# Performance work log

Hardware: AMD Instinct MI355X
Metric: run time of the kernel (lower is better)

Reference implementation:

```python
import jax, jax.numpy as jnp
import numpy as np

OUT, IN = 4096, 4096
BLOCK = 32
NBLK = IN // BLOCK  # 128


def setup_inputs() -> dict:
    key = jax.random.key(0)
    k1, k2, k3 = jax.random.split(key, 3)
    x = jax.random.normal(k1, (2, 2048, IN), dtype=jnp.float32)
    # per-block scales (GGUF stores fp16 scales; small magnitude typical)
    scales = jax.random.normal(k2, (OUT, NBLK), dtype=jnp.float32) * 0.01
    # int8 codes stored as unsigned 0..255; signed value = code - 128
    codes = jax.random.randint(k3, (OUT, NBLK, BLOCK), 0, 256, dtype=jnp.int32)
    return {"x": x, "scales": scales, "codes": codes}


def dequantize_q8_0(scales, codes):
    # scales: [out, nblk], codes: [out, nblk, 32] unsigned -> signed int8 semantics
    signed = codes.astype(jnp.float32) - 128.0
    w = scales[:, :, None] * signed            # [out, nblk, 32]
    return w.reshape(OUT, IN)                   # [out, in]


def reference(x, scales, codes):
    weight = dequantize_q8_0(scales, codes)     # [out, in]
    # nn.functional.linear: y = x @ weight.T
    return jnp.einsum("bsi,oi->bso", x, weight)
```

## Files before the change

### kernel.cpp

```cpp
#include <hip/hip_runtime.h>
#include <stdint.h>


#define M_DIM 4096
#define N_DIM 4096
#define K_DIM 4096
#define NT    64

typedef __attribute__((ext_vector_type(8))) short bf16x8;
typedef __attribute__((ext_vector_type(4))) float f32x4;

__device__ __forceinline__ unsigned short f32_to_bf16_rne(float f) {
    unsigned u = __float_as_uint(f);
    u += 0x7fffu + ((u >> 16) & 1u);
    return (unsigned short)(u >> 16);
}

__device__ __forceinline__ void load_lds16(const void* g, void* l) {
    __builtin_amdgcn_global_load_lds(
        (const __attribute__((address_space(1))) unsigned int*)g,
        (__attribute__((address_space(3))) unsigned int*)l, 16, 0, 0);
}

__global__ __launch_bounds__(256) void prologue_kernel(
        const int* __restrict__ codes, const float* __restrict__ scales,
        unsigned short* __restrict__ W,
        const float* __restrict__ x, unsigned short* __restrict__ xb) {
    const int bid = blockIdx.x;
    if (bid < 8192) {
        const int tid = bid * 256 + threadIdx.x;
        const int o   = tid >> 9;
        const int blk = (tid & 511) >> 2;
        const float s = scales[o * 128 + blk];
        const int4 c0 = ((const int4*)codes)[(size_t)tid * 2];
        const int4 c1 = ((const int4*)codes)[(size_t)tid * 2 + 1];
        union { unsigned short u[8]; uint4 v; } p;
        p.u[0] = f32_to_bf16_rne(s * (float)(c0.x - 128));
        p.u[1] = f32_to_bf16_rne(s * (float)(c0.y - 128));
        p.u[2] = f32_to_bf16_rne(s * (float)(c0.z - 128));
        p.u[3] = f32_to_bf16_rne(s * (float)(c0.w - 128));
        p.u[4] = f32_to_bf16_rne(s * (float)(c1.x - 128));
        p.u[5] = f32_to_bf16_rne(s * (float)(c1.y - 128));
        p.u[6] = f32_to_bf16_rne(s * (float)(c1.z - 128));
        p.u[7] = f32_to_bf16_rne(s * (float)(c1.w - 128));
        ((uint4*)W)[tid] = p.v;
    } else {
        const int tid = (bid - 8192) * 256 + threadIdx.x;
        const float4 f0 = ((const float4*)x)[(size_t)tid * 2];
        const float4 f1 = ((const float4*)x)[(size_t)tid * 2 + 1];
        union { unsigned short u[8]; uint4 v; } p;
        p.u[0] = f32_to_bf16_rne(f0.x); p.u[1] = f32_to_bf16_rne(f0.y);
        p.u[2] = f32_to_bf16_rne(f0.z); p.u[3] = f32_to_bf16_rne(f0.w);
        p.u[4] = f32_to_bf16_rne(f1.x); p.u[5] = f32_to_bf16_rne(f1.y);
        p.u[6] = f32_to_bf16_rne(f1.z); p.u[7] = f32_to_bf16_rne(f1.w);
        ((uint4*)xb)[tid] = p.v;
    }
}

#define BAR()   asm volatile("s_barrier" ::: "memory")
#define LGKM0() asm volatile("s_waitcnt lgkmcnt(0)" ::: "memory")
#define VMC(N)  asm volatile("s_waitcnt vmcnt(" #N ")" ::: "memory")

__global__ __launch_bounds__(512, 2) void gemm_8phase(
        const unsigned short* __restrict__ A,
        const unsigned short* __restrict__ B,
        float* __restrict__ C) {
    __shared__ unsigned short sA[2][2][256 * 32];
    __shared__ unsigned short sB[2][2][256 * 32];

    const int tid  = threadIdx.x;
    const int wave = tid >> 6;
    const int lane = tid & 63;

    const int bid  = blockIdx.x;
    const int xcd  = bid & 7;
    const int slot = bid >> 3;
    const int m0 = ((xcd >> 2) * 8 + (slot >> 2)) * 256;
    const int n0 = ((xcd & 3) * 4 + (slot & 3)) * 256;

    const int srow   = lane >> 2;
    const int schunk = (lane & 3) ^ ((lane >> 3) & 3);
    const unsigned short* Ag = A + (size_t)(m0 + wave * 32 + srow) * K_DIM + schunk * 8;
    const unsigned short* Bg = B + (size_t)(n0 + wave * 32 + srow) * K_DIM + schunk * 8;
    const int ldsW = wave * 1024;

    const int frow = lane & 15;
    const int quad = lane >> 4;
    const int wm = wave >> 2;
    const int wn = wave & 3;
    const int cswz = (quad ^ ((frow >> 1) & 3)) * 8;
    const int aOff = (wm * 128 + frow) * 32 + cswz;
    const int bOff = (wn * 64 + frow) * 32 + cswz;

    f32x4 acc[8][4] = {};
    bf16x8 a[8], b0, b1, b2, b3;

#define STG_A(BUF, KH, KT) do { \
        const unsigned short* s_ = Ag + (size_t)(KT) * 64 + (KH) * 32; \
        load_lds16(s_,                       &sA[BUF][KH][ldsW]); \
        load_lds16(s_ + (size_t)16 * K_DIM,  &sA[BUF][KH][ldsW + 512]); \
    } while (0)
#define STG_B(BUF, KH, KT) do { \
        const unsigned short* s_ = Bg + (size_t)(KT) * 64 + (KH) * 32; \
        load_lds16(s_,                       &sB[BUF][KH][ldsW]); \
        load_lds16(s_ + (size_t)16 * K_DIM,  &sB[BUF][KH][ldsW + 512]); \
    } while (0)
#define RD_A(BUF, KH) do { _Pragma("unroll") \
        for (int mt_ = 0; mt_ < 8; ++mt_) \
            a[mt_] = *(const bf16x8*)&sA[BUF][KH][aOff + mt_ * 512]; \
    } while (0)
#define RD_B2(BUF, KH, NB, R0, R1) do { \
        R0 = *(const bf16x8*)&sB[BUF][KH][bOff + (NB) * 512]; \
        R1 = *(const bf16x8*)&sB[BUF][KH][bOff + (NB + 1) * 512]; \
    } while (0)
#define MM2(NC, R0, R1) do { _Pragma("unroll") \
        for (int mt_ = 0; mt_ < 8; ++mt_) { \
            acc[mt_][NC]     = __builtin_amdgcn_mfma_f32_16x16x32_bf16(a[mt_], R0, acc[mt_][NC],     0, 0, 0); \
            acc[mt_][NC + 1] = __builtin_amdgcn_mfma_f32_16x16x32_bf16(a[mt_], R1, acc[mt_][NC + 1], 0, 0, 0); \
        } } while (0)

#define KTILE(BUF, OBUF, T, I1, I2, I3, I4, VMF) do { \
         \
        RD_A(BUF, 0); RD_B2(BUF, 0, 0, b0, b1); \
        if (I1) { STG_B(OBUF, 1, (T) + 1); } \
        BAR(); LGKM0(); __builtin_amdgcn_s_setprio(1); \
        MM2(0, b0, b1); \
        __builtin_amdgcn_s_setprio(0); BAR(); \
         \
        RD_B2(BUF, 0, 2, b2, b3); \
        if (I2) { STG_A(BUF, 0, (T) + 2); } \
        BAR(); LGKM0(); __builtin_amdgcn_s_setprio(1); \
        MM2(2, b2, b3); \
        __builtin_amdgcn_s_setprio(0); BAR(); \
         \
        RD_A(BUF, 1); RD_B2(BUF, 1, 0, b0, b1); \
        if (I3) { STG_B(BUF, 0, (T) + 2); } \
        BAR(); LGKM0(); __builtin_amdgcn_s_setprio(1); \
        MM2(0, b0, b1); \
        __builtin_amdgcn_s_setprio(0); BAR(); \
         \
        RD_B2(BUF, 1, 2, b2, b3); \
        if (I4) { STG_A(BUF, 1, (T) + 2); } \
        BAR(); LGKM0(); __builtin_amdgcn_s_setprio(1); \
        MM2(2, b2, b3); \
        __builtin_amdgcn_s_setprio(0); \
        VMF; BAR(); \
    } while (0)

    STG_A(0, 0, 0); STG_B(0, 0, 0); STG_A(0, 1, 0); STG_B(0, 1, 0);
    STG_A(1, 0, 1); STG_B(1, 0, 1); STG_A(1, 1, 1);
    VMC(6); BAR();

#pragma unroll 1
    for (int t2 = 0; t2 < 31; ++t2) {
        const int t = t2 * 2;
        KTILE(0, 1, t,     1, 1, 1, 1, VMC(6));
        KTILE(1, 0, t + 1, 1, 1, 1, 1, VMC(6));
    }
    KTILE(0, 1, 62, 1, 0, 0, 0, VMC(0));
    KTILE(1, 0, 63, 0, 0, 0, 0, (void)0);

    const size_t crow0 = (size_t)(m0 + wm * 128 + quad * 4);
    const int    ccol  = n0 + wn * 64 + frow;
#pragma unroll
    for (int mt = 0; mt < 8; ++mt)
#pragma unroll
        for (int nt = 0; nt < 4; ++nt)
#pragma unroll
            for (int r = 0; r < 4; ++r)
                C[(crow0 + mt * 16 + r) * N_DIM + ccol + nt * 16] = acc[mt][nt][r];

#undef STG_A
#undef STG_B
#undef RD_A
#undef RD_B2
#undef MM2
#undef KTILE
}

extern "C" void kernel_launch(void* const* d_in, const int* in_sizes, int n_in,
                              void* d_out, int out_size, void* d_ws, size_t ws_size,
                              hipStream_t stream) {
    const float* x      = (const float*)d_in[0];
    const float* scales = (const float*)d_in[1];
    const int*   codes  = (const int*)d_in[2];
    float* y = (float*)d_out;

    unsigned short* Wb = (unsigned short*)d_ws;
    unsigned short* xb = (unsigned short*)((char*)d_ws + (size_t)N_DIM * K_DIM * 2);

    prologue_kernel<<<16384, 256, 0, stream>>>(codes, scales, Wb, x, xb);

    gemm_8phase<<<256, 512, 0, stream>>>(xb, Wb, y);
}
```

Before: 293.4 us.

## Split MFMA phases by M-half to cut A-fragment registers; halve prologue work per thread

The GEMM inner phases now hold 4 A fragments and 4 B fragments instead of 8 A fragments plus 4 B fragments. Each phase computes a 4x4 MFMA block over one M-half, and the staging order of A/B tiles across phases is rearranged to match. The intent is to lower VGPR pressure and balance LDS reads per phase, at the cost of re-reading the B fragments per K-half. The prologue is also changed to process 4 elements per thread with twice as many blocks, which gives more parallelism but narrower 8-byte stores.

```diff
diff --git a/kernel.cpp b/kernel.cpp
--- a/kernel.cpp
+++ b/kernel.cpp
@@ -5,7 +5,6 @@
 #define M_DIM 4096
 #define N_DIM 4096
 #define K_DIM 4096
-#define NT    64
 
 typedef __attribute__((ext_vector_type(8))) short bf16x8;
 typedef __attribute__((ext_vector_type(4))) float f32x4;
@@ -27,33 +26,23 @@
         unsigned short* __restrict__ W,
         const float* __restrict__ x, unsigned short* __restrict__ xb) {
     const int bid = blockIdx.x;
-    if (bid < 8192) {
+    if (bid < 16384) {
         const int tid = bid * 256 + threadIdx.x;
-        const int o   = tid >> 9;
-        const int blk = (tid & 511) >> 2;
-        const float s = scales[o * 128 + blk];
-        const int4 c0 = ((const int4*)codes)[(size_t)tid * 2];
-        const int4 c1 = ((const int4*)codes)[(size_t)tid * 2 + 1];
-        union { unsigned short u[8]; uint4 v; } p;
-        p.u[0] = f32_to_bf16_rne(s * (float)(c0.x - 128));
-        p.u[1] = f32_to_bf16_rne(s * (float)(c0.y - 128));
-        p.u[2] = f32_to_bf16_rne(s * (float)(c0.z - 128));
-        p.u[3] = f32_to_bf16_rne(s * (float)(c0.w - 128));
-        p.u[4] = f32_to_bf16_rne(s * (float)(c1.x - 128));
-        p.u[5] = f32_to_bf16_rne(s * (float)(c1.y - 128));
-        p.u[6] = f32_to_bf16_rne(s * (float)(c1.z - 128));
-        p.u[7] = f32_to_bf16_rne(s * (float)(c1.w - 128));
-        ((uint4*)W)[tid] = p.v;
+        const float s = scales[tid >> 3];
+        const int4 c  = ((const int4*)codes)[tid];
+        union { unsigned short u[4]; uint2 v; } p;
+        p.u[0] = f32_to_bf16_rne(s * (float)(c.x - 128));
+        p.u[1] = f32_to_bf16_rne(s * (float)(c.y - 128));
+        p.u[2] = f32_to_bf16_rne(s * (float)(c.z - 128));
+        p.u[3] = f32_to_bf16_rne(s * (float)(c.w - 128));
+        ((uint2*)W)[tid] = p.v;
     } else {
-        const int tid = (bid - 8192) * 256 + threadIdx.x;
-        const float4 f0 = ((const float4*)x)[(size_t)tid * 2];
-        const float4 f1 = ((const float4*)x)[(size_t)tid * 2 + 1];
-        union { unsigned short u[8]; uint4 v; } p;
-        p.u[0] = f32_to_bf16_rne(f0.x); p.u[1] = f32_to_bf16_rne(f0.y);
-        p.u[2] = f32_to_bf16_rne(f0.z); p.u[3] = f32_to_bf16_rne(f0.w);
-        p.u[4] = f32_to_bf16_rne(f1.x); p.u[5] = f32_to_bf16_rne(f1.y);
-        p.u[6] = f32_to_bf16_rne(f1.z); p.u[7] = f32_to_bf16_rne(f1.w);
-        ((uint4*)xb)[tid] = p.v;
+        const int tid = (bid - 16384) * 256 + threadIdx.x;
+        const float4 f = ((const float4*)x)[tid];
+        union { unsigned short u[4]; uint2 v; } p;
+        p.u[0] = f32_to_bf16_rne(f.x); p.u[1] = f32_to_bf16_rne(f.y);
+        p.u[2] = f32_to_bf16_rne(f.z); p.u[3] = f32_to_bf16_rne(f.w);
+        ((uint2*)xb)[tid] = p.v;
     }
 }
 
@@ -93,7 +82,7 @@
     const int bOff = (wn * 64 + frow) * 32 + cswz;
 
     f32x4 acc[8][4] = {};
-    bf16x8 a[8], b0, b1, b2, b3;
+    bf16x8 a[4], b[4];
 
 #define STG_A(BUF, KH, KT) do { \
         const unsigned short* s_ = Ag + (size_t)(KT) * 64 + (KH) * 32; \
@@ -105,50 +94,51 @@
         load_lds16(s_,                       &sB[BUF][KH][ldsW]); \
         load_lds16(s_ + (size_t)16 * K_DIM,  &sB[BUF][KH][ldsW + 512]); \
     } while (0)
-#define RD_A(BUF, KH) do { _Pragma("unroll") \
-        for (int mt_ = 0; mt_ < 8; ++mt_) \
-            a[mt_] = *(const bf16x8*)&sA[BUF][KH][aOff + mt_ * 512]; \
+#define RD_A4(BUF, KH, MH) do { _Pragma("unroll") \
+        for (int i_ = 0; i_ < 4; ++i_) \
+            a[i_] = *(const bf16x8*)&sA[BUF][KH][aOff + ((MH) * 4 + i_) * 512]; \
     } while (0)
-#define RD_B2(BUF, KH, NB, R0, R1) do { \
-        R0 = *(const bf16x8*)&sB[BUF][KH][bOff + (NB) * 512]; \
-        R1 = *(const bf16x8*)&sB[BUF][KH][bOff + (NB + 1) * 512]; \
+#define RD_B4(BUF, KH) do { _Pragma("unroll") \
+        for (int i_ = 0; i_ < 4; ++i_) \
+            b[i_] = *(const bf16x8*)&sB[BUF][KH][bOff + i_ * 512]; \
     } while (0)
-#define MM2(NC, R0, R1) do { _Pragma("unroll") \
-        for (int mt_ = 0; mt_ < 8; ++mt_) { \
-            acc[mt_][NC]     = __builtin_amdgcn_mfma_f32_16x16x32_bf16(a[mt_], R0, acc[mt_][NC],     0, 0, 0); \
-            acc[mt_][NC + 1] = __builtin_amdgcn_mfma_f32_16x16x32_bf16(a[mt_], R1, acc[mt_][NC + 1], 0, 0, 0); \
+#define MM16(MH) do { _Pragma("unroll") \
+        for (int i_ = 0; i_ < 4; ++i_) { _Pragma("unroll") \
+            for (int n_ = 0; n_ < 4; ++n_) \
+                acc[(MH) * 4 + i_][n_] = __builtin_amdgcn_mfma_f32_16x16x32_bf16( \
+                    a[i_], b[n_], acc[(MH) * 4 + i_][n_], 0, 0, 0); \
         } } while (0)
 
 #define KTILE(BUF, OBUF, T, I1, I2, I3, I4, VMF) do { \
          \
-        RD_A(BUF, 0); RD_B2(BUF, 0, 0, b0, b1); \
-        if (I1) { STG_B(OBUF, 1, (T) + 1); } \
+        RD_A4(BUF, 0, 0); RD_B4(BUF, 0); \
+        if (I1) { STG_A(OBUF, 1, (T) + 1); } \
         BAR(); LGKM0(); __builtin_amdgcn_s_setprio(1); \
-        MM2(0, b0, b1); \
+        MM16(0); \
         __builtin_amdgcn_s_setprio(0); BAR(); \
          \
-        RD_B2(BUF, 0, 2, b2, b3); \
-        if (I2) { STG_A(BUF, 0, (T) + 2); } \
+        RD_A4(BUF, 0, 1); \
+        if (I2) { STG_B(BUF, 0, (T) + 2); } \
         BAR(); LGKM0(); __builtin_amdgcn_s_setprio(1); \
-        MM2(2, b2, b3); \
+        MM16(1); \
         __builtin_amdgcn_s_setprio(0); BAR(); \
          \
-        RD_A(BUF, 1); RD_B2(BUF, 1, 0, b0, b1); \
-        if (I3) { STG_B(BUF, 0, (T) + 2); } \
+        RD_A4(BUF, 1, 0); RD_B4(BUF, 1); \
+        if (I3) { STG_A(BUF, 0, (T) + 2); } \
         BAR(); LGKM0(); __builtin_amdgcn_s_setprio(1); \
-        MM2(0, b0, b1); \
+        MM16(0); \
         __builtin_amdgcn_s_setprio(0); BAR(); \
          \
-        RD_B2(BUF, 1, 2, b2, b3); \
-        if (I4) { STG_A(BUF, 1, (T) + 2); } \
+        RD_A4(BUF, 1, 1); \
+        if (I4) { STG_B(BUF, 1, (T) + 2); } \
         BAR(); LGKM0(); __builtin_amdgcn_s_setprio(1); \
-        MM2(2, b2, b3); \
+        MM16(1); \
         __builtin_amdgcn_s_setprio(0); \
         VMF; BAR(); \
     } while (0)
 
     STG_A(0, 0, 0); STG_B(0, 0, 0); STG_A(0, 1, 0); STG_B(0, 1, 0);
-    STG_A(1, 0, 1); STG_B(1, 0, 1); STG_A(1, 1, 1);
+    STG_B(1, 0, 1); STG_A(1, 0, 1); STG_B(1, 1, 1);
     VMC(6); BAR();
 
 #pragma unroll 1
@@ -172,9 +162,9 @@
 
 #undef STG_A
 #undef STG_B
-#undef RD_A
-#undef RD_B2
-#undef MM2
+#undef RD_A4
+#undef RD_B4
+#undef MM16
 #undef KTILE
 }
 
@@ -189,7 +179,7 @@
     unsigned short* Wb = (unsigned short*)d_ws;
     unsigned short* xb = (unsigned short*)((char*)d_ws + (size_t)N_DIM * K_DIM * 2);
 
-    prologue_kernel<<<16384, 256, 0, stream>>>(codes, scales, Wb, x, xb);
+    prologue_kernel<<<32768, 256, 0, stream>>>(codes, scales, Wb, x, xb);
 
     gemm_8phase<<<256, 512, 0, stream>>>(xb, Wb, y);
 }
```

Result: no change. 290.2 us (-1.1%).
